# Optimization experiments

Measured on AMD Instinct MI355X. Metric: run time of the kernel, lower is better.

The kernel has to match this reference:

```python
import jax, jax.numpy as jnp
import numpy as np

# dims matching init_kwargs
NC_IN, NC_OUT = 32, 32
M_IN, M_OUT = 3, 3          # to_order(degree)=2*d+1 with degree=1
NUM_FREQ = 3                # to_order(min(degree_in, degree_out))
EDGE_DIM, MID_DIM = 32, 64  # mid_dim = int(edge_dim * radial_mult)
RAD_OUT = NUM_FREQ * NC_IN * NC_OUT  # 3072
LN_EPS = 1e-5


def _layernorm(x, g, b):
    mu = jnp.mean(x, axis=-1, keepdims=True)
    var = jnp.var(x, axis=-1, keepdims=True)
    return (x - mu) * jax.lax.rsqrt(var + LN_EPS) * g + b


def setup_inputs() -> dict:
    key = jax.random.key(0)
    ks = jax.random.split(key, 8)
    B, N, K = 1, 1024, 32
    edges = jax.random.normal(ks[0], (B, N, K, EDGE_DIM), dtype=jnp.float32)
    feats = jax.random.normal(ks[1], (B, N, K, NC_IN, M_IN), dtype=jnp.float32)
    basis = jax.random.normal(ks[2], (B * N * K, M_IN, NUM_FREQ * M_OUT), dtype=jnp.float32)
    # radial MLP params (Linear -> LN -> GELU) x2, then Linear (no bias since dropout=0)
    s1 = 1.0 / np.sqrt(EDGE_DIM)
    s2 = 1.0 / np.sqrt(MID_DIM)
    W1 = jax.random.uniform(ks[3], (EDGE_DIM, MID_DIM), jnp.float32, -s1, s1)
    b1 = jnp.zeros((MID_DIM,), jnp.float32)
    g1 = jnp.ones((MID_DIM,), jnp.float32)
    beta1 = jnp.zeros((MID_DIM,), jnp.float32)
    W2 = jax.random.uniform(ks[4], (MID_DIM, MID_DIM), jnp.float32, -s2, s2)
    b2 = jnp.zeros((MID_DIM,), jnp.float32)
    g2 = jnp.ones((MID_DIM,), jnp.float32)
    beta2 = jnp.zeros((MID_DIM,), jnp.float32)
    W3 = jax.random.uniform(ks[5], (MID_DIM, RAD_OUT), jnp.float32, -s2, s2)
    return dict(edges=edges, feats=feats, basis=basis, W1=W1, b1=b1, g1=g1,
                beta1=beta1, W2=W2, b2=b2, g2=g2, beta2=beta2, W3=W3)


def reference(edges, feats, basis, W1, b1, g1, beta1, W2, b2, g2, beta2, W3):
    B, N, K = feats.shape[:3]
    E = B * N * K
    # radial MLP: (E, edge_dim) -> (E, nc_out * nc_in * num_freq)
    x = edges.reshape(E, EDGE_DIM)
    h = jax.nn.gelu(_layernorm(x @ W1 + b1, g1, beta1), approximate=False)
    h = jax.nn.gelu(_layernorm(h @ W2 + b2, g2, beta2), approximate=False)
    rw = (h @ W3).reshape(E, NC_OUT, NC_IN * NUM_FREQ)  # rearrange '(o i f)' then flatten
    # feats @ basis: (E, nc_in, m_in) @ (E, m_in, num_freq*m_out)
    f = feats.reshape(E, NC_IN, M_IN)
    tmp = jnp.matmul(f, basis).reshape(E, NC_IN * NUM_FREQ, M_OUT)
    out = jnp.matmul(rw, tmp)  # (E, nc_out, m_out)
    return out.reshape(B, N, K, NC_OUT, M_OUT)
```

## Files before the change

### kernel.cpp

```cpp
#include <hip/hip_runtime.h>
#include <cstdint>
#include <cstddef>

typedef __bf16 bf8 __attribute__((ext_vector_type(8)));
typedef float f32x4 __attribute__((ext_vector_type(4)));
typedef float f32x4u __attribute__((ext_vector_type(4), aligned(4)));
typedef float f32x3u __attribute__((ext_vector_type(3), aligned(4)));
typedef unsigned short us8 __attribute__((ext_vector_type(8)));
typedef unsigned short us4 __attribute__((ext_vector_type(4)));

__device__ __forceinline__ uint16_t f2b(float f) {
    uint32_t u = __builtin_bit_cast(uint32_t, f);
    u += 0x7FFFu + ((u >> 16) & 1u);
    return (uint16_t)(u >> 16);
}
__device__ __forceinline__ float b2f(uint16_t h) {
    uint32_t u = ((uint32_t)h) << 16;
    return __builtin_bit_cast(float, u);
}
__device__ __forceinline__ float gelu_fast(float y) {
    float y3 = y * y * y;
    float z2 = 1.5957691216f * (y + 0.044715f * y3);
    float u = __expf(-z2);
    return y * __builtin_amdgcn_rcpf(1.0f + u);
}

#define MFMA(a, b, c) __builtin_amdgcn_mfma_f32_16x16x32_bf16( \
    __builtin_bit_cast(bf8, (a)), __builtin_bit_cast(bf8, (b)), (c), 0, 0, 0)

__global__ void prep_weights(const float* __restrict__ W1,
                             const float* __restrict__ W2,
                             const float* __restrict__ W3,
                             uint16_t* __restrict__ wt) {
    __shared__ float tile[32][33];
    int bx = blockIdx.x;
    if (bx < 192) {
        int kb = (bx & 1) * 32;
        int jb = (bx >> 1) * 32;
        int tx = threadIdx.x & 31, ty = threadIdx.x >> 5;
        #pragma unroll
        for (int l = 0; l < 4; ++l)
            tile[ty + 8 * l][tx] = W3[(size_t)(kb + ty + 8 * l) * 3072 + jb + tx];
        __syncthreads();
        #pragma unroll
        for (int l = 0; l < 4; ++l) {
            int j = jb + ty + 8 * l;
            wt[6144 + (size_t)j * 64 + kb + tx] = f2b(tile[tx][ty + 8 * l]);
        }
    } else {
        int t = (bx - 192) * 256 + threadIdx.x;
        if (t < 2048) {
            int i = t >> 6, j = t & 63;
            wt[j * 32 + i] = f2b(W1[t]);
        } else {
            int t2 = t - 2048;
            int k = t2 >> 6, j = t2 & 63;
            wt[2048 + j * 64 + k] = f2b(W2[t2]);
        }
    }
}

__global__ __launch_bounds__(256, 2) void pairconv_main(
    const float* __restrict__ edges, const float* __restrict__ feats,
    const float* __restrict__ basis,
    const float* __restrict__ b1, const float* __restrict__ g1, const float* __restrict__ be1,
    const float* __restrict__ b2, const float* __restrict__ g2, const float* __restrict__ be2,
    const uint16_t* __restrict__ wt, float* __restrict__ out) {

    __shared__ __align__(16) uint16_t sh_tmp[64 * 384];
    __shared__ __align__(16) uint16_t sh_h[64 * 64];
    __shared__ __align__(16) uint16_t sh_h1[4][16 * 64];

    const int tid = threadIdx.x;
    const int e0 = blockIdx.x * 64;
    const int lane = tid & 63, w = tid >> 6;
    const int n = lane & 15, q = lane >> 4;

    const int eb = e0 + w * 16;
    f32x4 ex0 = *(const f32x4*)(edges + (size_t)(eb + n) * 32 + q * 8);
    f32x4 ex1 = *(const f32x4*)(edges + (size_t)(eb + n) * 32 + q * 8 + 4);

    #pragma unroll
    for (int it = 0; it < 8; ++it) {
        int idx = tid + it * 256;
        int e = idx >> 5, i = idx & 31;
        f32x3u fv = *(const f32x3u*)(feats + ((size_t)(e0 + e) * 32 + i) * 3);
        const float* bpp = basis + (size_t)(e0 + e) * 27;
        float bp[27];
        #pragma unroll
        for (int v = 0; v < 6; ++v) {
            f32x4u t = *(const f32x4u*)(bpp + v * 4);
            bp[v * 4] = t[0]; bp[v * 4 + 1] = t[1]; bp[v * 4 + 2] = t[2]; bp[v * 4 + 3] = t[3];
        }
        bp[24] = bpp[24]; bp[25] = bpp[25]; bp[26] = bpp[26];
        int sw = e & 7;
        #pragma unroll
        for (int f = 0; f < 3; ++f) {
            int c = i * 3 + f;
            int u = c >> 1;
            us4 pk;
            #pragma unroll
            for (int m = 0; m < 3; ++m) {
                float v = fv[0] * bp[f * 3 + m] + fv[1] * bp[9 + f * 3 + m] + fv[2] * bp[18 + f * 3 + m];
                pk[m] = f2b(v);
            }
            pk[3] = 0;
            *(us4*)&sh_tmp[e * 384 + ((u ^ sw) << 3) + (c & 1) * 4] = pk;
        }
    }

    {
        us8 bx;
        #pragma unroll
        for (int j = 0; j < 4; ++j) { bx[j] = f2b(ex0[j]); bx[4 + j] = f2b(ex1[j]); }
        f32x4 acc[4];
        #pragma unroll
        for (int mt = 0; mt < 4; ++mt) {
            us8 a = *(const us8*)(wt + (mt * 16 + n) * 32 + q * 8);
            f32x4 z = {0.f, 0.f, 0.f, 0.f};
            acc[mt] = MFMA(a, bx, z);
        }
        float v[4][4];
        float s1 = 0.f, s2 = 0.f;
        #pragma unroll
        for (int mt = 0; mt < 4; ++mt) {
            f32x4 bb = *(const f32x4*)&b1[mt * 16 + q * 4];
            #pragma unroll
            for (int r = 0; r < 4; ++r) {
                float x = acc[mt][r] + bb[r];
                v[mt][r] = x; s1 += x; s2 += x * x;
            }
        }
        s1 += __shfl_xor(s1, 16, 64); s1 += __shfl_xor(s1, 32, 64);
        s2 += __shfl_xor(s2, 16, 64); s2 += __shfl_xor(s2, 32, 64);
        float mean = s1 * (1.f / 64.f);
        float var  = s2 * (1.f / 64.f) - mean * mean;
        float rs = __builtin_amdgcn_rsqf(var + 1e-5f);
        #pragma unroll
        for (int mt = 0; mt < 4; ++mt) {
            f32x4 gg = *(const f32x4*)&g1[mt * 16 + q * 4];
            f32x4 be = *(const f32x4*)&be1[mt * 16 + q * 4];
            us4 pk;
            #pragma unroll
            for (int r = 0; r < 4; ++r) {
                float y = (v[mt][r] - mean) * rs * gg[r] + be[r];
                pk[r] = f2b(gelu_fast(y));
            }
            int kq = mt * 2 + (q >> 1);
            *(us4*)&sh_h1[w][n * 64 + ((kq ^ (n & 7)) << 3) + (q & 1) * 4] = pk;
        }
    }
    {
        us8 bh0 = *(const us8*)&sh_h1[w][n * 64 + ((q ^ (n & 7)) << 3)];
        us8 bh1 = *(const us8*)&sh_h1[w][n * 64 + (((4 + q) ^ (n & 7)) << 3)];
        f32x4 acc[4];
        #pragma unroll
        for (int mt = 0; mt < 4; ++mt) {
            us8 a0 = *(const us8*)(wt + 2048 + (mt * 16 + n) * 64 + q * 8);
            us8 a1 = *(const us8*)(wt + 2048 + (mt * 16 + n) * 64 + 32 + q * 8);
            f32x4 z = {0.f, 0.f, 0.f, 0.f};
            acc[mt] = MFMA(a0, bh0, z);
            acc[mt] = MFMA(a1, bh1, acc[mt]);
        }
        float v[4][4]; float s1 = 0.f, s2 = 0.f;
        #pragma unroll
        for (int mt = 0; mt < 4; ++mt) {
            f32x4 bb = *(const f32x4*)&b2[mt * 16 + q * 4];
            #pragma unroll
            for (int r = 0; r < 4; ++r) {
                float x = acc[mt][r] + bb[r];
                v[mt][r] = x; s1 += x; s2 += x * x;
            }
        }
        s1 += __shfl_xor(s1, 16, 64); s1 += __shfl_xor(s1, 32, 64);
        s2 += __shfl_xor(s2, 16, 64); s2 += __shfl_xor(s2, 32, 64);
        float mean = s1 * (1.f / 64.f);
        float var  = s2 * (1.f / 64.f) - mean * mean;
        float rs = __builtin_amdgcn_rsqf(var + 1e-5f);
        #pragma unroll
        for (int mt = 0; mt < 4; ++mt) {
            f32x4 gg = *(const f32x4*)&g2[mt * 16 + q * 4];
            f32x4 be = *(const f32x4*)&be2[mt * 16 + q * 4];
            us4 pk;
            #pragma unroll
            for (int r = 0; r < 4; ++r) {
                float y = (v[mt][r] - mean) * rs * gg[r] + be[r];
                pk[r] = f2b(gelu_fast(y));
            }
            int e = w * 16 + n;
            int kq = mt * 2 + (q >> 1);
            *(us4*)&sh_h[e * 64 + ((kq ^ (e & 7)) << 3) + (q & 1) * 4] = pk;
        }
    }
    __syncthreads();

    {
        const uint16_t* w3t = wt + 6144;
        us8 bh[4][2];
        #pragma unroll
        for (int nt = 0; nt < 4; ++nt) {
            int e = nt * 16 + n;
            bh[nt][0] = *(const us8*)&sh_h[e * 64 + ((q ^ (e & 7)) << 3)];
            bh[nt][1] = *(const us8*)&sh_h[e * 64 + (((4 + q) ^ (e & 7)) << 3)];
        }
        const int ob = w * 8;
        #pragma unroll 1
        for (int oc = 0; oc < 2; ++oc) {
            float p[4][4][3];
            #pragma unroll
            for (int a = 0; a < 4; ++a)
                #pragma unroll
                for (int b = 0; b < 4; ++b)
                    #pragma unroll
                    for (int m = 0; m < 3; ++m) p[a][b][m] = 0.f;

            #pragma unroll 1
            for (int mt = 0; mt < 6; ++mt) {
                float ftmp[4][4][3];
                #pragma unroll
                for (int nt = 0; nt < 4; ++nt) {
                    int e = nt * 16 + n;
                    int u0 = mt * 8 + q * 2;
                    int sw = e & 7;
                    us8 t0 = *(const us8*)&sh_tmp[e * 384 + ((u0 ^ sw) << 3)];
                    us8 t1 = *(const us8*)&sh_tmp[e * 384 + (((u0 + 1) ^ sw) << 3)];
                    #pragma unroll
                    for (int m = 0; m < 3; ++m) {
                        ftmp[nt][0][m] = b2f(t0[m]);
                        ftmp[nt][1][m] = b2f(t0[4 + m]);
                        ftmp[nt][2][m] = b2f(t1[m]);
                        ftmp[nt][3][m] = b2f(t1[4 + m]);
                    }
                }
                #pragma unroll
                for (int op = 0; op < 4; ++op) {
                    int o = ob + oc * 4 + op;
                    const uint16_t* ap = w3t + (size_t)(o * 96 + mt * 16 + n) * 64 + q * 8;
                    us8 a0 = *(const us8*)ap;
                    us8 a1 = *(const us8*)(ap + 32);
                    #pragma unroll
                    for (int nt = 0; nt < 4; ++nt) {
                        f32x4 z = {0.f, 0.f, 0.f, 0.f};
                        f32x4 acc = MFMA(a0, bh[nt][0], z);
                        acc = MFMA(a1, bh[nt][1], acc);
                        #pragma unroll
                        for (int r = 0; r < 4; ++r)
                            #pragma unroll
                            for (int m = 0; m < 3; ++m)
                                p[nt][op][m] += acc[r] * ftmp[nt][r][m];
                    }
                }
            }
            #pragma unroll
            for (int nt = 0; nt < 4; ++nt) {
                #pragma unroll
                for (int op = 0; op < 4; ++op) {
                    int o = ob + oc * 4 + op;
                    float v0 = p[nt][op][0], v1 = p[nt][op][1], v2 = p[nt][op][2];
                    v0 += __shfl_xor(v0, 16, 64); v0 += __shfl_xor(v0, 32, 64);
                    v1 += __shfl_xor(v1, 16, 64); v1 += __shfl_xor(v1, 32, 64);
                    v2 += __shfl_xor(v2, 16, 64); v2 += __shfl_xor(v2, 32, 64);
                    float val = (q == 0) ? v0 : ((q == 1) ? v1 : v2);
                    if (q < 3)
                        out[(size_t)(e0 + nt * 16 + n) * 96 + o * 3 + q] = val;
                }
            }
        }
    }
}

extern "C" void kernel_launch(void* const* d_in, const int* in_sizes, int n_in,
                              void* d_out, int out_size, void* d_ws, size_t ws_size,
                              hipStream_t stream) {
    const float* edges = (const float*)d_in[0];
    const float* feats = (const float*)d_in[1];
    const float* basis = (const float*)d_in[2];
    const float* W1  = (const float*)d_in[3];
    const float* b1  = (const float*)d_in[4];
    const float* g1  = (const float*)d_in[5];
    const float* be1 = (const float*)d_in[6];
    const float* W2  = (const float*)d_in[7];
    const float* b2  = (const float*)d_in[8];
    const float* g2  = (const float*)d_in[9];
    const float* be2 = (const float*)d_in[10];
    const float* W3  = (const float*)d_in[11];
    uint16_t* wt = (uint16_t*)d_ws;
    float* out = (float*)d_out;

    const int E = in_sizes[0] / 32;
    hipLaunchKernelGGL(prep_weights, dim3(216), dim3(256), 0, stream, W1, W2, W3, wt);
    hipLaunchKernelGGL(pairconv_main, dim3(E / 64), dim3(256), 0, stream,
                       edges, feats, basis, b1, g1, be1, b2, g2, be2, wt, out);
}
```

Before: 130.4 us.

## Shrink blocks to 32 edges, repack tmp as bf16 pairs, use packed conversions

Halves the block to 128 threads handling 32 edges, so each wave now covers 16 output channels over 2 edge tiles instead of 8 channels over 4 tiles. The tmp buffer is stored as packed bf16 pairs plus a separate third component, which cuts shared-memory footprint and padding and allows packed-float FMA accumulation. W3 fragments are hoisted ahead of the MFMA loop, and bf16 conversions use the hardware packed convert where it is available. The intent is higher occupancy and less LDS and VALU work, at the cost of reading W3 more often per edge, since each block covers fewer edges.

```diff
diff --git a/kernel.cpp b/kernel.cpp
--- a/kernel.cpp
+++ b/kernel.cpp
@@ -4,10 +4,13 @@
 
 typedef __bf16 bf8 __attribute__((ext_vector_type(8)));
 typedef float f32x4 __attribute__((ext_vector_type(4)));
+typedef float f32x2 __attribute__((ext_vector_type(2)));
 typedef float f32x4u __attribute__((ext_vector_type(4), aligned(4)));
 typedef float f32x3u __attribute__((ext_vector_type(3), aligned(4)));
 typedef unsigned short us8 __attribute__((ext_vector_type(8)));
 typedef unsigned short us4 __attribute__((ext_vector_type(4)));
+typedef unsigned int u32x4 __attribute__((ext_vector_type(4)));
+typedef unsigned int u32x2 __attribute__((ext_vector_type(2)));
 
 __device__ __forceinline__ uint16_t f2b(float f) {
     uint32_t u = __builtin_bit_cast(uint32_t, f);
@@ -17,6 +20,22 @@
 __device__ __forceinline__ float b2f(uint16_t h) {
     uint32_t u = ((uint32_t)h) << 16;
     return __builtin_bit_cast(float, u);
+}
+#if __has_builtin(__builtin_amdgcn_cvt_pk_bf16_f32)
+__device__ __forceinline__ uint32_t pkbf(float a, float b) {
+    auto r = __builtin_amdgcn_cvt_pk_bf16_f32(a, b);
+    return __builtin_bit_cast(uint32_t, r);
+}
+#else
+__device__ __forceinline__ uint32_t pkbf(float a, float b) {
+    return (uint32_t)f2b(a) | ((uint32_t)f2b(b) << 16);
+}
+#endif
+__device__ __forceinline__ f32x2 up01(uint32_t d) {
+    f32x2 r;
+    r[0] = __builtin_bit_cast(float, d << 16);
+    r[1] = __builtin_bit_cast(float, d & 0xffff0000u);
+    return r;
 }
 __device__ __forceinline__ float gelu_fast(float y) {
     float y3 = y * y * y;
@@ -60,19 +79,19 @@
     }
 }
 
-__global__ __launch_bounds__(256, 2) void pairconv_main(
+__global__ __launch_bounds__(128, 3) void pairconv_main(
     const float* __restrict__ edges, const float* __restrict__ feats,
     const float* __restrict__ basis,
     const float* __restrict__ b1, const float* __restrict__ g1, const float* __restrict__ be1,
     const float* __restrict__ b2, const float* __restrict__ g2, const float* __restrict__ be2,
     const uint16_t* __restrict__ wt, float* __restrict__ out) {
 
-    __shared__ __align__(16) uint16_t sh_tmp[64 * 384];
-    __shared__ __align__(16) uint16_t sh_h[64 * 64];
-    __shared__ __align__(16) uint16_t sh_h1[4][16 * 64];
+    __shared__ __align__(16) uint32_t sh_t01[32 * 100];
+    __shared__ __align__(16) uint16_t sh_t2[32 * 104];
+    __shared__ __align__(16) uint16_t sh_h[2][16 * 64];
 
     const int tid = threadIdx.x;
-    const int e0 = blockIdx.x * 64;
+    const int e0 = blockIdx.x * 32;
     const int lane = tid & 63, w = tid >> 6;
     const int n = lane & 15, q = lane >> 4;
 
@@ -82,7 +101,7 @@
 
     #pragma unroll
     for (int it = 0; it < 8; ++it) {
-        int idx = tid + it * 256;
+        int idx = tid + it * 128;
         int e = idx >> 5, i = idx & 31;
         f32x3u fv = *(const f32x3u*)(feats + ((size_t)(e0 + e) * 32 + i) * 3);
         const float* bpp = basis + (size_t)(e0 + e) * 27;
@@ -93,26 +112,25 @@
             bp[v * 4] = t[0]; bp[v * 4 + 1] = t[1]; bp[v * 4 + 2] = t[2]; bp[v * 4 + 3] = t[3];
         }
         bp[24] = bpp[24]; bp[25] = bpp[25]; bp[26] = bpp[26];
-        int sw = e & 7;
         #pragma unroll
         for (int f = 0; f < 3; ++f) {
             int c = i * 3 + f;
-            int u = c >> 1;
-            us4 pk;
-            #pragma unroll
-            for (int m = 0; m < 3; ++m) {
-                float v = fv[0] * bp[f * 3 + m] + fv[1] * bp[9 + f * 3 + m] + fv[2] * bp[18 + f * 3 + m];
-                pk[m] = f2b(v);
-            }
-            pk[3] = 0;
-            *(us4*)&sh_tmp[e * 384 + ((u ^ sw) << 3) + (c & 1) * 4] = pk;
+            float v0 = fv[0] * bp[f * 3 + 0] + fv[1] * bp[9 + f * 3 + 0] + fv[2] * bp[18 + f * 3 + 0];
+            float v1 = fv[0] * bp[f * 3 + 1] + fv[1] * bp[9 + f * 3 + 1] + fv[2] * bp[18 + f * 3 + 1];
+            float v2 = fv[0] * bp[f * 3 + 2] + fv[1] * bp[9 + f * 3 + 2] + fv[2] * bp[18 + f * 3 + 2];
+            sh_t01[e * 100 + c] = pkbf(v0, v1);
+            sh_t2[e * 104 + c]  = (uint16_t)pkbf(v2, v2);
         }
     }
 
     {
         us8 bx;
-        #pragma unroll
-        for (int j = 0; j < 4; ++j) { bx[j] = f2b(ex0[j]); bx[4 + j] = f2b(ex1[j]); }
+        {
+            u32x4 bxp;
+            bxp[0] = pkbf(ex0[0], ex0[1]); bxp[1] = pkbf(ex0[2], ex0[3]);
+            bxp[2] = pkbf(ex1[0], ex1[1]); bxp[3] = pkbf(ex1[2], ex1[3]);
+            bx = __builtin_bit_cast(us8, bxp);
+        }
         f32x4 acc[4];
         #pragma unroll
         for (int mt = 0; mt < 4; ++mt) {
@@ -140,19 +158,18 @@
         for (int mt = 0; mt < 4; ++mt) {
             f32x4 gg = *(const f32x4*)&g1[mt * 16 + q * 4];
             f32x4 be = *(const f32x4*)&be1[mt * 16 + q * 4];
-            us4 pk;
-            #pragma unroll
-            for (int r = 0; r < 4; ++r) {
-                float y = (v[mt][r] - mean) * rs * gg[r] + be[r];
-                pk[r] = f2b(gelu_fast(y));
-            }
+            float y0 = gelu_fast((v[mt][0] - mean) * rs * gg[0] + be[0]);
+            float y1 = gelu_fast((v[mt][1] - mean) * rs * gg[1] + be[1]);
+            float y2 = gelu_fast((v[mt][2] - mean) * rs * gg[2] + be[2]);
+            float y3 = gelu_fast((v[mt][3] - mean) * rs * gg[3] + be[3]);
+            u32x2 pk; pk[0] = pkbf(y0, y1); pk[1] = pkbf(y2, y3);
             int kq = mt * 2 + (q >> 1);
-            *(us4*)&sh_h1[w][n * 64 + ((kq ^ (n & 7)) << 3) + (q & 1) * 4] = pk;
+            *(u32x2*)&sh_h[w][n * 64 + ((kq ^ (n & 7)) << 3) + (q & 1) * 4] = pk;
         }
     }
     {
-        us8 bh0 = *(const us8*)&sh_h1[w][n * 64 + ((q ^ (n & 7)) << 3)];
-        us8 bh1 = *(const us8*)&sh_h1[w][n * 64 + (((4 + q) ^ (n & 7)) << 3)];
+        us8 bh0 = *(const us8*)&sh_h[w][n * 64 + ((q ^ (n & 7)) << 3)];
+        us8 bh1 = *(const us8*)&sh_h[w][n * 64 + (((4 + q) ^ (n & 7)) << 3)];
         f32x4 acc[4];
         #pragma unroll
         for (int mt = 0; mt < 4; ++mt) {
@@ -181,82 +198,79 @@
         for (int mt = 0; mt < 4; ++mt) {
             f32x4 gg = *(const f32x4*)&g2[mt * 16 + q * 4];
             f32x4 be = *(const f32x4*)&be2[mt * 16 + q * 4];
-            us4 pk;
-            #pragma unroll
-            for (int r = 0; r < 4; ++r) {
-                float y = (v[mt][r] - mean) * rs * gg[r] + be[r];
-                pk[r] = f2b(gelu_fast(y));
-            }
-            int e = w * 16 + n;
+            float y0 = gelu_fast((v[mt][0] - mean) * rs * gg[0] + be[0]);
+            float y1 = gelu_fast((v[mt][1] - mean) * rs * gg[1] + be[1]);
+            float y2 = gelu_fast((v[mt][2] - mean) * rs * gg[2] + be[2]);
+            float y3 = gelu_fast((v[mt][3] - mean) * rs * gg[3] + be[3]);
+            u32x2 pk; pk[0] = pkbf(y0, y1); pk[1] = pkbf(y2, y3);
             int kq = mt * 2 + (q >> 1);
-            *(us4*)&sh_h[e * 64 + ((kq ^ (e & 7)) << 3) + (q & 1) * 4] = pk;
+            *(u32x2*)&sh_h[w][n * 64 + ((kq ^ (n & 7)) << 3) + (q & 1) * 4] = pk;
         }
     }
     __syncthreads();
 
     {
         const uint16_t* w3t = wt + 6144;
-        us8 bh[4][2];
-        #pragma unroll
-        for (int nt = 0; nt < 4; ++nt) {
-            int e = nt * 16 + n;
-            bh[nt][0] = *(const us8*)&sh_h[e * 64 + ((q ^ (e & 7)) << 3)];
-            bh[nt][1] = *(const us8*)&sh_h[e * 64 + (((4 + q) ^ (e & 7)) << 3)];
-        }
-        const int ob = w * 8;
+        us8 bh[2][2];
+        #pragma unroll
+        for (int nt = 0; nt < 2; ++nt) {
+            bh[nt][0] = *(const us8*)&sh_h[nt][n * 64 + ((q ^ (n & 7)) << 3)];
+            bh[nt][1] = *(const us8*)&sh_h[nt][n * 64 + (((4 + q) ^ (n & 7)) << 3)];
+        }
         #pragma unroll 1
-        for (int oc = 0; oc < 2; ++oc) {
-            float p[4][4][3];
+        for (int oc = 0; oc < 4; ++oc) {
+            f32x2 p01[4][2];
+            float p2v[4][2];
             #pragma unroll
-            for (int a = 0; a < 4; ++a)
-                #pragma unroll
-                for (int b = 0; b < 4; ++b)
-                    #pragma unroll
-                    for (int m = 0; m < 3; ++m) p[a][b][m] = 0.f;
+            for (int op = 0; op < 4; ++op)
+                #pragma unroll
+                for (int nt = 0; nt < 2; ++nt) {
+                    p01[op][nt] = (f32x2){0.f, 0.f}; p2v[op][nt] = 0.f;
+                }
 
             #pragma unroll 1
             for (int mt = 0; mt < 6; ++mt) {
-                float ftmp[4][4][3];
-                #pragma unroll
-                for (int nt = 0; nt < 4; ++nt) {
+                us8 a[4][2];
+                const uint16_t* apb = w3t +
+                    (size_t)((w * 16 + oc * 4) * 96 + mt * 16 + n) * 64 + q * 8;
+                #pragma unroll
+                for (int op = 0; op < 4; ++op) {
+                    a[op][0] = *(const us8*)(apb + (size_t)op * 6144);
+                    a[op][1] = *(const us8*)(apb + (size_t)op * 6144 + 32);
+                }
+                f32x2 f01[2][4]; float fm2[2][4];
+                #pragma unroll
+                for (int nt = 0; nt < 2; ++nt) {
                     int e = nt * 16 + n;
-                    int u0 = mt * 8 + q * 2;
-                    int sw = e & 7;
-                    us8 t0 = *(const us8*)&sh_tmp[e * 384 + ((u0 ^ sw) << 3)];
-                    us8 t1 = *(const us8*)&sh_tmp[e * 384 + (((u0 + 1) ^ sw) << 3)];
+                    u32x4 d  = *(const u32x4*)&sh_t01[e * 100 + mt * 16 + q * 4];
+                    us4 t2   = *(const us4*)&sh_t2[e * 104 + mt * 16 + q * 4];
                     #pragma unroll
-                    for (int m = 0; m < 3; ++m) {
-                        ftmp[nt][0][m] = b2f(t0[m]);
-                        ftmp[nt][1][m] = b2f(t0[4 + m]);
-                        ftmp[nt][2][m] = b2f(t1[m]);
-                        ftmp[nt][3][m] = b2f(t1[4 + m]);
+                    for (int r = 0; r < 4; ++r) {
+                        f01[nt][r] = up01(d[r]);
+                        fm2[nt][r] = b2f(t2[r]);
                     }
                 }
                 #pragma unroll
                 for (int op = 0; op < 4; ++op) {
-                    int o = ob + oc * 4 + op;
-                    const uint16_t* ap = w3t + (size_t)(o * 96 + mt * 16 + n) * 64 + q * 8;
-                    us8 a0 = *(const us8*)ap;
-                    us8 a1 = *(const us8*)(ap + 32);
                     #pragma unroll
-                    for (int nt = 0; nt < 4; ++nt) {
+                    for (int nt = 0; nt < 2; ++nt) {
                         f32x4 z = {0.f, 0.f, 0.f, 0.f};
-                        f32x4 acc = MFMA(a0, bh[nt][0], z);
-                        acc = MFMA(a1, bh[nt][1], acc);
+                        f32x4 acc = MFMA(a[op][0], bh[nt][0], z);
+                        acc = MFMA(a[op][1], bh[nt][1], acc);
                         #pragma unroll
-                        for (int r = 0; r < 4; ++r)
-                            #pragma unroll
-                            for (int m = 0; m < 3; ++m)
-                                p[nt][op][m] += acc[r] * ftmp[nt][r][m];
+                        for (int r = 0; r < 4; ++r) {
+                            p01[op][nt] += f01[nt][r] * acc[r];
+                            p2v[op][nt] += fm2[nt][r] * acc[r];
+                        }
                     }
                 }
             }
             #pragma unroll
-            for (int nt = 0; nt < 4; ++nt) {
+            for (int nt = 0; nt < 2; ++nt) {
                 #pragma unroll
                 for (int op = 0; op < 4; ++op) {
-                    int o = ob + oc * 4 + op;
-                    float v0 = p[nt][op][0], v1 = p[nt][op][1], v2 = p[nt][op][2];
+                    int o = w * 16 + oc * 4 + op;
+                    float v0 = p01[op][nt][0], v1 = p01[op][nt][1], v2 = p2v[op][nt];
                     v0 += __shfl_xor(v0, 16, 64); v0 += __shfl_xor(v0, 32, 64);
                     v1 += __shfl_xor(v1, 16, 64); v1 += __shfl_xor(v1, 32, 64);
                     v2 += __shfl_xor(v2, 16, 64); v2 += __shfl_xor(v2, 32, 64);
@@ -289,6 +303,6 @@
 
     const int E = in_sizes[0] / 32;
     hipLaunchKernelGGL(prep_weights, dim3(216), dim3(256), 0, stream, W1, W2, W3, wt);
-    hipLaunchKernelGGL(pairconv_main, dim3(E / 64), dim3(256), 0, stream,
+    hipLaunchKernelGGL(pairconv_main, dim3(E / 32), dim3(128), 0, stream,
                        edges, feats, basis, b1, g1, be1, b2, g2, be2, wt, out);
 }
```

Result: slower. 144.8 us (+11.1%).
